# Kernel tuning notes

Hardware: AMD Instinct MI355X
Metric: run time of the kernel (lower is better)

Reference implementation:

```python
import jax, jax.numpy as jnp
import numpy as np

B, C, L = 8, 256, 2048        # batch, query_dim, seq len
HEADS, DIM_HEAD = 4, 32
HIDDEN = HEADS * DIM_HEAD      # 128
EPS = 1e-05
SCALE = DIM_HEAD ** -0.5


def setup_inputs() -> dict:
    key = jax.random.key(0)
    ks = jax.random.split(key, 8)
    s_in = 1.0 / np.sqrt(C)
    s_h = 1.0 / np.sqrt(HIDDEN)
    return {
        "x": jax.random.normal(ks[0], (B, C, L), dtype=jnp.float32),
        "g": jnp.ones((1, C, 1), dtype=jnp.float32),
        "b": jnp.zeros((1, C, 1), dtype=jnp.float32),
        "Wq": jax.random.normal(ks[1], (HIDDEN, C), dtype=jnp.float32) * s_in,
        "Wk": jax.random.normal(ks[2], (HIDDEN, C), dtype=jnp.float32) * s_in,
        "Wv": jax.random.normal(ks[3], (HIDDEN, C), dtype=jnp.float32) * s_in,
        "Wo": jax.random.normal(ks[4], (C, HIDDEN), dtype=jnp.float32) * s_h,
        "bo": jnp.zeros((C,), dtype=jnp.float32),
    }


def reference(x, g, b, Wq, Wk, Wv, Wo, bo):
    og_x = x
    # channel-dim LayerNorm (dim=1), biased variance
    mean = jnp.mean(x, axis=1, keepdims=True)
    var = jnp.var(x, axis=1, keepdims=True)
    xn = (x - mean) / jnp.sqrt(var + EPS) * g + b          # [B, C, L]
    xt = jnp.transpose(xn, (0, 2, 1))                      # [B, L, C]
    # QKV projections (self-attention: context = normed x)
    q = xt @ Wq.T                                          # [B, L, HIDDEN]
    k = xt @ Wk.T
    v = xt @ Wv.T
    # b (h c) d layout: [B, HEADS, DIM_HEAD, L]
    split = lambda t: jnp.transpose(t, (0, 2, 1)).reshape(B, HEADS, DIM_HEAD, L)
    q, k, v = split(q), split(k), split(v)
    # scores over head-channel dim c -> [B, H, L, L]
    qk = jnp.einsum('bhcd,bhce->bhde', q, k) * SCALE
    attn = jax.nn.softmax(qk, axis=-1)
    out = jnp.einsum('bhde,bhce->bhcd', attn, v)           # [B, H, DIM_HEAD, L]
    out = out.reshape(B, HIDDEN, L)
    # 1x1 Conv1d: hidden -> query_dim
    y = jnp.einsum('oc,bcl->bol', Wo, out) + bo[None, :, None]
    return y + og_x
```

## Files before the change

### kernel.cpp

```cpp
#include <hip/hip_runtime.h>
#include <math.h>

#define BB_ 8
#define CC_ 256
#define LL_ 2048
#define HEADS_ 4
#define DHEAD_ 32
#define HID_ 128
#define EPS_ 1e-5f
#define SCALE_ 0.17677669529663687f
#define K1_ (SCALE_ * 1.44269504088896f)

typedef short v8s  __attribute__((ext_vector_type(8)));
typedef float v4f  __attribute__((ext_vector_type(4)));
typedef float v16f __attribute__((ext_vector_type(16)));
typedef unsigned v4u __attribute__((ext_vector_type(4)));

__device__ inline short f2bf(float x) {
    union { float f; unsigned u; } a; a.f = x;
    unsigned r = a.u + 0x7fffu + ((a.u >> 16) & 1u);
    return (short)(r >> 16);
}
__device__ inline unsigned fbits(float x) { union { float f; unsigned u; } a; a.f = x; return a.u; }

__global__ __launch_bounds__(256) void k_prep(
    const float* __restrict__ Wq, const float* __restrict__ Wk, const float* __restrict__ Wv,
    const float* __restrict__ Wo, const float* __restrict__ g, const float* __restrict__ bvec,
    short* __restrict__ wqkv, short* __restrict__ wo, float2* __restrict__ gb)
{
    __shared__ float red0[256], red1[256];
    const int blk = blockIdx.x, c = threadIdx.x;
    if (blk < 384) {
        const float* W; int oo; float scale = 1.f;
        if (blk < 128)      { W = Wq; oo = blk;       scale = K1_; }
        else if (blk < 256) { W = Wk; oo = blk - 128; }
        else                { W = Wv; oo = blk - 256; }
        float w  = W[oo * 256 + c] * scale;
        float wg = w * g[c];
        wqkv[blk * 256 + c] = f2bf(wg);
        red0[c] = wg;
        red1[c] = w * bvec[c];
        __syncthreads();
        for (int s = 128; s > 0; s >>= 1) {
            if (c < s) { red0[c] += red0[c + s]; red1[c] += red1[c + s]; }
            __syncthreads();
        }
        if (c == 0) gb[blk] = make_float2(red0[0], red1[0]);
    } else {
        int i2 = (blk - 384) * 256 + c;
        wo[i2] = f2bf(Wo[i2]);
    }
}

__global__ __launch_bounds__(512) void k_ln_qkv(
    const float* __restrict__ x, const short* __restrict__ wqkv, const float2* __restrict__ gb,
    short* __restrict__ q, short* __restrict__ k, short* __restrict__ v)
{
    __shared__ float xn[CC_ * 33];
    __shared__ short xnT[32 * 264];
    __shared__ short st2[128 * 48];
    __shared__ float ps_[8 * 32], ps2_[8 * 32];
    __shared__ float rs_s[32], rsmu_s[32];
    const int b   = blockIdx.y;
    const int l0  = blockIdx.x * 32;
    const int tid = threadIdx.x;
    const int wave = tid >> 6, lane = tid & 63;

    {
        const int ls = tid & 31;
        float s = 0.f, s2 = 0.f;
        #pragma unroll
        for (int kk = 0; kk < 16; ++kk) {
            int c = (tid >> 5) + 16 * kk;
            float t = x[((size_t)b * CC_ + c) * LL_ + l0 + ls];
            xn[c * 33 + ls] = t;
            s += t; s2 += t * t;
        }
        s  += __shfl_xor(s, 32, 64);
        s2 += __shfl_xor(s2, 32, 64);
        if (lane < 32) { ps_[wave * 32 + lane] = s; ps2_[wave * 32 + lane] = s2; }
    }
    __syncthreads();
    if (tid < 32) {
        float s = 0.f, s2 = 0.f;
        #pragma unroll
        for (int p = 0; p < 8; ++p) { s += ps_[p * 32 + tid]; s2 += ps2_[p * 32 + tid]; }
        float mean = s * (1.f / CC_);
        float var  = s2 * (1.f / CC_) - mean * mean;
        float rs   = rsqrtf(var + EPS_);
        rs_s[tid]   = rs;
        rsmu_s[tid] = rs * mean;
    }
    for (int idx = tid; idx < 32 * 128; idx += 512) {
        int ls = idx >> 7, cc = idx & 127;
        int c0 = 2 * cc;
        xnT[ls * 264 + c0]     = f2bf(xn[c0 * 33 + ls]);
        xnT[ls * 264 + c0 + 1] = f2bf(xn[(c0 + 1) * 33 + ls]);
    }
    __syncthreads();

    const int n = lane & 15, quad = lane >> 4;
    const int rowbase = (wave >> 2) * 16;
    const int colbase = (wave & 3) * 96;

    v4f acc[6];
    #pragma unroll
    for (int ct = 0; ct < 6; ++ct) acc[ct] = (v4f){0.f, 0.f, 0.f, 0.f};

    #pragma unroll
    for (int ks = 0; ks < 8; ++ks) {
        const v8s af = *(const v8s*)(xnT + (rowbase + n) * 264 + ks * 32 + quad * 8);
        #pragma unroll
        for (int ct = 0; ct < 6; ++ct) {
            const v8s bfrag = *(const v8s*)(wqkv + (size_t)(colbase + ct * 16 + n) * 256 + ks * 32 + quad * 8);
            acc[ct] = __builtin_amdgcn_mfma_f32_16x16x32_bf16(af, bfrag, acc[ct], 0, 0, 0);
        }
    }
    __syncthreads();

    float rsv[4], rmv[4];
    #pragma unroll
    for (int r = 0; r < 4; ++r) {
        int l = rowbase + quad * 4 + r;
        rsv[r] = rs_s[l]; rmv[r] = rsmu_s[l];
    }
    #pragma unroll
    for (int ct = 0; ct < 6; ++ct) {
        int o = colbase + ct * 16 + n;
        float2 gbo = gb[o];
        #pragma unroll
        for (int r = 0; r < 4; ++r) {
            int l = rowbase + quad * 4 + r;
            float val = rsv[r] * acc[ct][r] - rmv[r] * gbo.x + gbo.y;
            if (o < 256)      xnT[l * 264 + o] = f2bf(val);
            else              st2[(o - 256) * 48 + l] = f2bf(val);
        }
    }
    __syncthreads();

    {
        int u = tid;
        int h = u >> 7, rest = u & 127;
        int l = rest >> 2, dg = rest & 3;
        size_t bh = (size_t)b * HEADS_ + h;
        v8s qv = *(const v8s*)(xnT + l * 264 + h * 32 + dg * 8);
        *(v8s*)(q + (bh * LL_ + l0 + l) * DHEAD_ + dg * 8) = qv;
        v8s kv = *(const v8s*)(xnT + l * 264 + 128 + h * 32 + dg * 8);
        *(v8s*)(k + (bh * LL_ + l0 + l) * DHEAD_ + dg * 8) = kv;

        int op = u >> 2, lg = u & 3;
        v8s vv = *(const v8s*)(st2 + op * 48 + lg * 8);
        int h2 = op >> 5, d = op & 31;
        *(v8s*)(v + (((size_t)b * HEADS_ + h2) * DHEAD_ + d) * LL_ + l0 + lg * 8) = vv;
    }
}

#define CHK_ 256
__global__ __launch_bounds__(256) void k_attn(
    const short* __restrict__ q, const short* __restrict__ k, const short* __restrict__ v,
    short* __restrict__ ao)
{
    __shared__ short Kb[CHK_ * 40];
    __shared__ short Vb[32 * 264];
    const int bh   = blockIdx.y;
    const int b    = bh >> 2, h = bh & 3;
    const int tid  = threadIdx.x;
    const int wave = tid >> 6, lane = tid & 63;
    const int m    = lane & 31;
    const int half = lane >> 5;
    const size_t kvbase = (size_t)bh * LL_ * DHEAD_;
    const size_t vbase  = (size_t)bh * DHEAD_ * LL_;

    const int q0 = blockIdx.x * 128 + wave * 32;

    const v8s qf0 = *(const v8s*)(q + kvbase + (size_t)(q0 + m) * DHEAD_ + half * 8);
    const v8s qf1 = *(const v8s*)(q + kvbase + (size_t)(q0 + m) * DHEAD_ + 16 + half * 8);

    v16f O = {};
    float psum = 0.f;

    for (int kc = 0; kc < LL_; kc += CHK_) {
        __syncthreads();
        {
            const short* src = k + kvbase + (size_t)(kc + tid) * DHEAD_;
            short* dst = Kb + tid * 40;
            #pragma unroll
            for (int j = 0; j < 4; ++j)
                *(v8s*)(dst + j * 8) = *(const v8s*)(src + j * 8);
        }
        {
            const int col = (tid & 31) * 8, dr = tid >> 5;
            #pragma unroll
            for (int p = 0; p < 4; ++p) {
                int d = p * 8 + dr;
                *(v8s*)(Vb + d * 264 + col) =
                    *(const v8s*)(v + vbase + (size_t)d * LL_ + kc + col);
            }
        }
        __syncthreads();

        #pragma unroll
        for (int ktl = 0; ktl < CHK_; ktl += 32) {
            const v8s kf0 = *(const v8s*)(Kb + (ktl + m) * 40 + half * 8);
            const v8s kf1 = *(const v8s*)(Kb + (ktl + m) * 40 + 16 + half * 8);
            v16f S = __builtin_amdgcn_mfma_f32_32x32x16_bf16(kf0, qf0, (v16f){}, 0, 0, 0);
            S      = __builtin_amdgcn_mfma_f32_32x32x16_bf16(kf1, qf1, S,        0, 0, 0);

            const v8s vf0 = *(const v8s*)(Vb + m * 264 + ktl + half * 8);
            const v8s vf1 = *(const v8s*)(Vb + m * 264 + ktl + 16 + half * 8);

            unsigned e[8];
            #pragma unroll
            for (int i = 0; i < 8; ++i) {
                float pa = __builtin_amdgcn_exp2f(S[2 * i]);
                float pb = __builtin_amdgcn_exp2f(S[2 * i + 1]);
                psum += pa + pb;
                e[i] = __builtin_amdgcn_perm(fbits(pb) + 0x8000u, fbits(pa) + 0x8000u, 0x07060302u);
            }
            v4u f1, f2;
#if __has_builtin(__builtin_amdgcn_permlane32_swap)
            {
                auto r02 = __builtin_amdgcn_permlane32_swap(e[0], e[2], false, false);
                auto r13 = __builtin_amdgcn_permlane32_swap(e[1], e[3], false, false);
                auto r46 = __builtin_amdgcn_permlane32_swap(e[4], e[6], false, false);
                auto r57 = __builtin_amdgcn_permlane32_swap(e[5], e[7], false, false);
                f1 = (v4u){r02[0], r13[0], r02[1], r13[1]};
                f2 = (v4u){r46[0], r57[0], r46[1], r57[1]};
            }
#else
            {
                unsigned o0 = __shfl_xor(e[0], 32, 64), o1 = __shfl_xor(e[1], 32, 64);
                unsigned o2 = __shfl_xor(e[2], 32, 64), o3 = __shfl_xor(e[3], 32, 64);
                unsigned o4 = __shfl_xor(e[4], 32, 64), o5 = __shfl_xor(e[5], 32, 64);
                unsigned o6 = __shfl_xor(e[6], 32, 64), o7 = __shfl_xor(e[7], 32, 64);
                f1 = half ? (v4u){o2, o3, e[2], e[3]} : (v4u){e[0], e[1], o0, o1};
                f2 = half ? (v4u){o6, o7, e[6], e[7]} : (v4u){e[4], e[5], o4, o5};
            }
#endif
            O = __builtin_amdgcn_mfma_f32_32x32x16_bf16(__builtin_bit_cast(v8s, f1), vf0, O, 0, 0, 0);
            O = __builtin_amdgcn_mfma_f32_32x32x16_bf16(__builtin_bit_cast(v8s, f2), vf1, O, 0, 0, 0);
        }
    }

    psum += __shfl_xor(psum, 32, 64);
    float invden = 1.f / psum;
    #pragma unroll
    for (int r = 0; r < 16; ++r) {
        int qr = (r & 3) + 8 * (r >> 2) + 4 * half;
        float inv = __shfl(invden, qr, 64);
        int row = q0 + qr;
        ao[((size_t)b * LL_ + row) * HID_ + h * DHEAD_ + m] = f2bf(O[r] * inv);
    }
}

__global__ __launch_bounds__(256) void k_oproj(
    const short* __restrict__ ao, const short* __restrict__ wo, const float* __restrict__ bo,
    const float* __restrict__ x, float* __restrict__ out)
{
    const int b = blockIdx.z;
    const int l0 = blockIdx.x * 16;
    const int obase = blockIdx.y * 8;
    const int tid = threadIdx.x;
    const int wave = tid >> 6, lane = tid & 63;
    const int n = lane & 15, quad = lane >> 4;

    v8s bf[4];
    #pragma unroll
    for (int ks = 0; ks < 4; ++ks)
        bf[ks] = *(const v8s*)(ao + ((size_t)b * LL_ + l0 + n) * HID_ + ks * 32 + quad * 8);

    #pragma unroll
    for (int oi_ = 0; oi_ < 2; ++oi_) {
        int ot = obase + wave * 2 + oi_;
        v4f acc = {0.f, 0.f, 0.f, 0.f};
        #pragma unroll
        for (int ks = 0; ks < 4; ++ks) {
            const v8s af = *(const v8s*)(wo + (size_t)(ot * 16 + n) * HID_ + ks * 32 + quad * 8);
            acc = __builtin_amdgcn_mfma_f32_16x16x32_bf16(af, bf[ks], acc, 0, 0, 0);
        }
        #pragma unroll
        for (int r = 0; r < 4; ++r) {
            int o = ot * 16 + quad * 4 + r;
            size_t oi = ((size_t)b * CC_ + o) * LL_ + l0 + n;
            out[oi] = acc[r] + bo[o] + x[oi];
        }
    }
}

extern "C" void kernel_launch(void* const* d_in, const int* in_sizes, int n_in,
                              void* d_out, int out_size, void* d_ws, size_t ws_size,
                              hipStream_t stream) {
    const float* x  = (const float*)d_in[0];
    const float* g  = (const float*)d_in[1];
    const float* bv = (const float*)d_in[2];
    const float* Wq = (const float*)d_in[3];
    const float* Wk = (const float*)d_in[4];
    const float* Wv = (const float*)d_in[5];
    const float* Wo = (const float*)d_in[6];
    const float* bo = (const float*)d_in[7];
    float* out = (float*)d_out;

    const size_t qkv_elems = (size_t)BB_ * HEADS_ * LL_ * DHEAD_;
    short* q    = (short*)d_ws;
    short* k    = q + qkv_elems;
    short* v    = k + qkv_elems;
    short* ao   = v + qkv_elems;
    short* wqkv = ao + qkv_elems;
    short* wo   = wqkv + 384 * 256;
    float2* gb  = (float2*)(wo + 256 * 128);

    k_prep  <<<dim3(512), dim3(256), 0, stream>>>(Wq, Wk, Wv, Wo, g, bv, wqkv, wo, gb);
    k_ln_qkv<<<dim3(LL_ / 32, BB_), dim3(512), 0, stream>>>(x, wqkv, gb, q, k, v);
    k_attn  <<<dim3(LL_ / 128, BB_ * HEADS_), dim3(256), 0, stream>>>(q, k, v, ao);
    k_oproj <<<dim3(LL_ / 16, 2, BB_), dim3(256), 0, stream>>>(ao, wo, bo, x, out);
}
```

Before: 166.7 us.

## Streamline prep reduction, LN staging, and widen out-projection to 32x32 MFMA

The weight-prep reduction now uses wave shuffles instead of a shared-memory tree with many barriers. The LN+QKV kernel drops the fp32 staging buffer and writes bf16 pairs straight into the transposed tile, and each thread computes its own row statistics in place of a separate serial step. The output projection uses 32x32x16 MFMA tiles over 32 positions, so each block covers twice as many positions and reuses more of each load. These changes cut LDS traffic and barriers, at the cost of more registers per thread in the projection kernel.

```diff
diff --git a/kernel.cpp b/kernel.cpp
--- a/kernel.cpp
+++ b/kernel.cpp
@@ -28,8 +28,9 @@
     const float* __restrict__ Wo, const float* __restrict__ g, const float* __restrict__ bvec,
     short* __restrict__ wqkv, short* __restrict__ wo, float2* __restrict__ gb)
 {
-    __shared__ float red0[256], red1[256];
+    __shared__ float red0[4], red1[4];
     const int blk = blockIdx.x, c = threadIdx.x;
+    const int wave = c >> 6, lane = c & 63;
     if (blk < 384) {
         const float* W; int oo; float scale = 1.f;
         if (blk < 128)      { W = Wq; oo = blk;       scale = K1_; }
@@ -38,14 +39,17 @@
         float w  = W[oo * 256 + c] * scale;
         float wg = w * g[c];
         wqkv[blk * 256 + c] = f2bf(wg);
-        red0[c] = wg;
-        red1[c] = w * bvec[c];
+        float r0 = wg, r1 = w * bvec[c];
+        #pragma unroll
+        for (int off = 1; off < 64; off <<= 1) {
+            r0 += __shfl_xor(r0, off, 64);
+            r1 += __shfl_xor(r1, off, 64);
+        }
+        if (lane == 0) { red0[wave] = r0; red1[wave] = r1; }
         __syncthreads();
-        for (int s = 128; s > 0; s >>= 1) {
-            if (c < s) { red0[c] += red0[c + s]; red1[c] += red1[c + s]; }
-            __syncthreads();
-        }
-        if (c == 0) gb[blk] = make_float2(red0[0], red1[0]);
+        if (c == 0)
+            gb[blk] = make_float2(red0[0] + red0[1] + red0[2] + red0[3],
+                                  red1[0] + red1[1] + red1[2] + red1[3]);
     } else {
         int i2 = (blk - 384) * 256 + c;
         wo[i2] = f2bf(Wo[i2]);
@@ -56,11 +60,9 @@
     const float* __restrict__ x, const short* __restrict__ wqkv, const float2* __restrict__ gb,
     short* __restrict__ q, short* __restrict__ k, short* __restrict__ v)
 {
-    __shared__ float xn[CC_ * 33];
     __shared__ short xnT[32 * 264];
     __shared__ short st2[128 * 48];
     __shared__ float ps_[8 * 32], ps2_[8 * 32];
-    __shared__ float rs_s[32], rsmu_s[32];
     const int b   = blockIdx.y;
     const int l0  = blockIdx.x * 32;
     const int tid = threadIdx.x;
@@ -68,61 +70,53 @@
 
     {
         const int ls = tid & 31;
+        const int cg = tid >> 5;
         float s = 0.f, s2 = 0.f;
         #pragma unroll
-        for (int kk = 0; kk < 16; ++kk) {
-            int c = (tid >> 5) + 16 * kk;
-            float t = x[((size_t)b * CC_ + c) * LL_ + l0 + ls];
-            xn[c * 33 + ls] = t;
-            s += t; s2 += t * t;
+        for (int kk = 0; kk < 8; ++kk) {
+            int c = 2 * cg + 32 * kk;
+            float t0 = x[((size_t)b * CC_ + c) * LL_ + l0 + ls];
+            float t1 = x[((size_t)b * CC_ + c + 1) * LL_ + l0 + ls];
+            s += t0 + t1; s2 += t0 * t0 + t1 * t1;
+            unsigned pk = (unsigned short)f2bf(t0) | ((unsigned)(unsigned short)f2bf(t1) << 16);
+            *(unsigned*)(xnT + ls * 264 + c) = pk;
         }
         s  += __shfl_xor(s, 32, 64);
         s2 += __shfl_xor(s2, 32, 64);
         if (lane < 32) { ps_[wave * 32 + lane] = s; ps2_[wave * 32 + lane] = s2; }
     }
     __syncthreads();
-    if (tid < 32) {
+
+    const int n = lane & 15, quad = lane >> 4;
+    const int rowbase = (wave >> 2) * 16;
+    const int colbase = (wave & 3) * 96;
+
+    v4f acc[6];
+    #pragma unroll
+    for (int ct = 0; ct < 6; ++ct) acc[ct] = (v4f){0.f, 0.f, 0.f, 0.f};
+
+    #pragma unroll
+    for (int ks = 0; ks < 8; ++ks) {
+        const v8s af = *(const v8s*)(xnT + (rowbase + n) * 264 + ks * 32 + quad * 8);
+        #pragma unroll
+        for (int ct = 0; ct < 6; ++ct) {
+            const v8s bfrag = *(const v8s*)(wqkv + (size_t)(colbase + ct * 16 + n) * 256 + ks * 32 + quad * 8);
+            acc[ct] = __builtin_amdgcn_mfma_f32_16x16x32_bf16(af, bfrag, acc[ct], 0, 0, 0);
+        }
+    }
+    __syncthreads();
+
+    float rsv[4], rmv[4];
+    #pragma unroll
+    for (int r = 0; r < 4; ++r) {
+        int l = rowbase + quad * 4 + r;
         float s = 0.f, s2 = 0.f;
         #pragma unroll
-        for (int p = 0; p < 8; ++p) { s += ps_[p * 32 + tid]; s2 += ps2_[p * 32 + tid]; }
+        for (int p = 0; p < 8; ++p) { s += ps_[p * 32 + l]; s2 += ps2_[p * 32 + l]; }
         float mean = s * (1.f / CC_);
         float var  = s2 * (1.f / CC_) - mean * mean;
         float rs   = rsqrtf(var + EPS_);
-        rs_s[tid]   = rs;
-        rsmu_s[tid] = rs * mean;
-    }
-    for (int idx = tid; idx < 32 * 128; idx += 512) {
-        int ls = idx >> 7, cc = idx & 127;
-        int c0 = 2 * cc;
-        xnT[ls * 264 + c0]     = f2bf(xn[c0 * 33 + ls]);
-        xnT[ls * 264 + c0 + 1] = f2bf(xn[(c0 + 1) * 33 + ls]);
-    }
-    __syncthreads();
-
-    const int n = lane & 15, quad = lane >> 4;
-    const int rowbase = (wave >> 2) * 16;
-    const int colbase = (wave & 3) * 96;
-
-    v4f acc[6];
-    #pragma unroll
-    for (int ct = 0; ct < 6; ++ct) acc[ct] = (v4f){0.f, 0.f, 0.f, 0.f};
-
-    #pragma unroll
-    for (int ks = 0; ks < 8; ++ks) {
-        const v8s af = *(const v8s*)(xnT + (rowbase + n) * 264 + ks * 32 + quad * 8);
-        #pragma unroll
-        for (int ct = 0; ct < 6; ++ct) {
-            const v8s bfrag = *(const v8s*)(wqkv + (size_t)(colbase + ct * 16 + n) * 256 + ks * 32 + quad * 8);
-            acc[ct] = __builtin_amdgcn_mfma_f32_16x16x32_bf16(af, bfrag, acc[ct], 0, 0, 0);
-        }
-    }
-    __syncthreads();
-
-    float rsv[4], rmv[4];
-    #pragma unroll
-    for (int r = 0; r < 4; ++r) {
-        int l = rowbase + quad * 4 + r;
-        rsv[r] = rs_s[l]; rmv[r] = rsmu_s[l];
+        rsv[r] = rs; rmv[r] = rs * mean;
     }
     #pragma unroll
     for (int ct = 0; ct < 6; ++ct) {
@@ -258,32 +252,29 @@
     const float* __restrict__ x, float* __restrict__ out)
 {
     const int b = blockIdx.z;
-    const int l0 = blockIdx.x * 16;
-    const int obase = blockIdx.y * 8;
+    const int l0 = blockIdx.x * 32;
     const int tid = threadIdx.x;
     const int wave = tid >> 6, lane = tid & 63;
-    const int n = lane & 15, quad = lane >> 4;
-
-    v8s bf[4];
-    #pragma unroll
-    for (int ks = 0; ks < 4; ++ks)
-        bf[ks] = *(const v8s*)(ao + ((size_t)b * LL_ + l0 + n) * HID_ + ks * 32 + quad * 8);
-
-    #pragma unroll
-    for (int oi_ = 0; oi_ < 2; ++oi_) {
-        int ot = obase + wave * 2 + oi_;
-        v4f acc = {0.f, 0.f, 0.f, 0.f};
-        #pragma unroll
-        for (int ks = 0; ks < 4; ++ks) {
-            const v8s af = *(const v8s*)(wo + (size_t)(ot * 16 + n) * HID_ + ks * 32 + quad * 8);
-            acc = __builtin_amdgcn_mfma_f32_16x16x32_bf16(af, bf[ks], acc, 0, 0, 0);
-        }
-        #pragma unroll
-        for (int r = 0; r < 4; ++r) {
-            int o = ot * 16 + quad * 4 + r;
-            size_t oi = ((size_t)b * CC_ + o) * LL_ + l0 + n;
-            out[oi] = acc[r] + bo[o] + x[oi];
-        }
+    const int m = lane & 31, half = lane >> 5;
+    const int o0 = blockIdx.y * 128 + wave * 32;
+
+    v8s bf[8];
+    #pragma unroll
+    for (int ks = 0; ks < 8; ++ks)
+        bf[ks] = *(const v8s*)(ao + ((size_t)b * LL_ + l0 + m) * HID_ + ks * 16 + half * 8);
+
+    v16f acc = {};
+    #pragma unroll
+    for (int ks = 0; ks < 8; ++ks) {
+        const v8s af = *(const v8s*)(wo + (size_t)(o0 + m) * HID_ + ks * 16 + half * 8);
+        acc = __builtin_amdgcn_mfma_f32_32x32x16_bf16(af, bf[ks], acc, 0, 0, 0);
+    }
+
+    #pragma unroll
+    for (int r = 0; r < 16; ++r) {
+        int o = o0 + (r & 3) + 8 * (r >> 2) + 4 * half;
+        size_t oi = ((size_t)b * CC_ + o) * LL_ + l0 + m;
+        out[oi] = acc[r] + bo[o] + x[oi];
     }
 }
 
@@ -312,5 +303,5 @@
     k_prep  <<<dim3(512), dim3(256), 0, stream>>>(Wq, Wk, Wv, Wo, g, bv, wqkv, wo, gb);
     k_ln_qkv<<<dim3(LL_ / 32, BB_), dim3(512), 0, stream>>>(x, wqkv, gb, q, k, v);
     k_attn  <<<dim3(LL_ / 128, BB_ * HEADS_), dim3(256), 0, stream>>>(q, k, v, ao);
-    k_oproj <<<dim3(LL_ / 16, 2, BB_), dim3(256), 0, stream>>>(ao, wo, bo, x, out);
-}
+    k_oproj <<<dim3(LL_ / 32, 2, BB_), dim3(256), 0, stream>>>(ao, wo, bo, x, out);
+}
```

Result: faster. 163.2 us (-2.1%).
